# Kernel tuning notes

Hardware: AMD Instinct MI355X
Metric: run time of the kernel (lower is better)

Reference implementation:

```python
import jax, jax.numpy as jnp
import numpy as np

EPS = 1e-5
INIT_PERSIST = 0.5

def _layernorm(x):
    mu = jnp.mean(x, axis=-1, keepdims=True)
    var = jnp.var(x, axis=-1, keepdims=True)
    return (x - mu) / jnp.sqrt(var + EPS)

def setup_inputs() -> dict:
    key = jax.random.key(0)
    k1, k2, k3, k4 = jax.random.split(key, 4)
    B, T, D, N = 8, 48, 512, 1024
    return {
        "x_seq": jax.random.normal(k1, (B, T, D), dtype=jnp.float32),
        "targets": jax.random.normal(k2, (B, T, D), dtype=jnp.float32),
        "E": jax.random.normal(k3, (D, N), dtype=jnp.float32) * 0.1,
        "Dy": jax.random.normal(k4, (N, D), dtype=jnp.float32) * 0.1,
        "mix_param": jnp.zeros((), dtype=jnp.float32),
    }

def reference(x_seq, targets, E, Dy, mix_param):
    B, T, D = x_seq.shape
    N = E.shape[1]
    alpha = jax.nn.sigmoid(mix_param)

    # initial states: persist = 0.5*I, transition = 0
    Gp0 = jnp.broadcast_to(jnp.eye(N, dtype=x_seq.dtype) * INIT_PERSIST, (B, N, N))
    Gt0 = jnp.zeros((B, N, N), dtype=x_seq.dtype)

    # target for step t's update is targets[:, t+1]; last step has no update
    tgt_next = jnp.concatenate([targets[:, 1:, :], jnp.zeros_like(targets[:, :1, :])], axis=1)
    do_upd = jnp.arange(T) < (T - 1)  # [T] bool

    xs = (jnp.swapaxes(x_seq, 0, 1), jnp.swapaxes(tgt_next, 0, 1), do_upd)

    def step(carry, inp):
        Gp, Gt = carry
        x_t, tn_t, upd = inp
        xn = jax.nn.relu(_layernorm(x_t @ E))          # [B, N]
        r_p = jnp.einsum("bn,bnm->bm", xn, Gp)
        r_t = jnp.einsum("bn,bnm->bm", xn, Gt)
        y = jax.nn.relu((alpha * r_p + (1.0 - alpha) * r_t) @ Dy)  # [B, D]
        tn = jax.nn.relu(_layernorm(tn_t @ E))          # [B, N]
        Gt_new = jnp.maximum(Gt, 0.5 * xn[:, :, None] * tn[:, None, :])
        Gp_new = jnp.maximum(Gp, 0.5 * xn[:, :, None] * xn[:, None, :])
        Gt = jnp.where(upd, Gt_new, Gt)
        Gp = jnp.where(upd, Gp_new, Gp)
        return (Gp, Gt), y

    _, ys = jax.lax.scan(step, (Gp0, Gt0), xs)
    return jnp.swapaxes(ys, 0, 1)  # [B, T, D]
```

## Files before the change

### kernel.cpp

```cpp
#include <hip/hip_runtime.h>
#include <math.h>

#define BB 8
#define TT 48
#define DD 512
#define NN 1024

__global__ __launch_bounds__(256) void k_gemm_z(const float* __restrict__ x,
                                                const float* __restrict__ tg,
                                                const float* __restrict__ E,
                                                float* __restrict__ z_x,
                                                float* __restrict__ z_t) {
    int rt = blockIdx.x, ct = blockIdx.y;
    int tid = threadIdx.x;
    int tr = tid >> 4;
    int tc = tid & 15;
    int row0 = rt * 32;
    int col0 = ct * 64;

    __shared__ float As[32][16];
    __shared__ float Es[16][64];

    int e2 = tid * 2;
    int sr = e2 >> 4;
    int sk0 = e2 & 15;
    int gr_s = row0 + sr;
    const float* srow;
    if (gr_s < BB * TT) {
        srow = x + (size_t)gr_s * DD;
    } else {
        int s = gr_s - BB * TT + 1;
        if (s > BB * TT - 1) s = BB * TT - 1;
        srow = tg + (size_t)s * DD;
    }

    int se = tid >> 4;
    int sc0 = (tid & 15) * 4;
    const float* erow = E + col0 + sc0;

    float4 acc0 = make_float4(0.f, 0.f, 0.f, 0.f);
    float4 acc1 = make_float4(0.f, 0.f, 0.f, 0.f);

    for (int d0 = 0; d0 < DD; d0 += 16) {
        float2 xv = *reinterpret_cast<const float2*>(srow + d0 + sk0);
        float4 ev = *reinterpret_cast<const float4*>(erow + (size_t)(d0 + se) * NN);
        __syncthreads();
        As[sr][sk0] = xv.x;
        As[sr][sk0 + 1] = xv.y;
        *reinterpret_cast<float4*>(&Es[se][sc0]) = ev;
        __syncthreads();
#pragma unroll
        for (int k = 0; k < 16; k++) {
            float a0 = As[tr][k];
            float a1 = As[tr + 16][k];
            float4 e = *reinterpret_cast<const float4*>(&Es[k][tc * 4]);
            acc0.x = fmaf(a0, e.x, acc0.x);
            acc0.y = fmaf(a0, e.y, acc0.y);
            acc0.z = fmaf(a0, e.z, acc0.z);
            acc0.w = fmaf(a0, e.w, acc0.w);
            acc1.x = fmaf(a1, e.x, acc1.x);
            acc1.y = fmaf(a1, e.y, acc1.y);
            acc1.z = fmaf(a1, e.z, acc1.z);
            acc1.w = fmaf(a1, e.w, acc1.w);
        }
    }

    int gr0 = row0 + tr, gr1 = row0 + tr + 16;
    int cbase = col0 + tc * 4;
    if (gr0 < BB * TT)
        *reinterpret_cast<float4*>(z_x + (size_t)gr0 * NN + cbase) = acc0;
    else
        *reinterpret_cast<float4*>(z_t + (size_t)(gr0 - BB * TT) * NN + cbase) = acc0;
    if (gr1 < BB * TT)
        *reinterpret_cast<float4*>(z_x + (size_t)gr1 * NN + cbase) = acc1;
    else
        *reinterpret_cast<float4*>(z_t + (size_t)(gr1 - BB * TT) * NN + cbase) = acc1;
}

__global__ __launch_bounds__(256) void k_ln(const float* __restrict__ z_x,
                                            const float* __restrict__ z_t,
                                            float* __restrict__ xn,
                                            float* __restrict__ tn) {
    int bt = blockIdx.x;
    int t = bt % TT;
    int tid = threadIdx.x;
    __shared__ float rs_[256], rq_[256];

    const float* src = z_x + (size_t)bt * NN;
    float v0 = src[tid], v1 = src[tid + 256], v2 = src[tid + 512], v3 = src[tid + 768];
    rs_[tid] = v0 + v1 + v2 + v3;
    rq_[tid] = v0 * v0 + v1 * v1 + v2 * v2 + v3 * v3;
    __syncthreads();
    for (int off = 128; off > 0; off >>= 1) {
        if (tid < off) { rs_[tid] += rs_[tid + off]; rq_[tid] += rq_[tid + off]; }
        __syncthreads();
    }
    float mu = rs_[0] * (1.f / NN);
    float var = rq_[0] * (1.f / NN) - mu * mu;
    float rstd = rsqrtf(var + 1e-5f);
    float* xrow = xn + (size_t)bt * NN;
    xrow[tid]       = fmaxf((v0 - mu) * rstd, 0.f);
    xrow[tid + 256] = fmaxf((v1 - mu) * rstd, 0.f);
    xrow[tid + 512] = fmaxf((v2 - mu) * rstd, 0.f);
    xrow[tid + 768] = fmaxf((v3 - mu) * rstd, 0.f);
    __syncthreads();

    float* trow = tn + (size_t)bt * NN;
    if (t < TT - 1) {
        const float* s2 = z_t + (size_t)bt * NN;
        float u0 = s2[tid], u1 = s2[tid + 256], u2 = s2[tid + 512], u3 = s2[tid + 768];
        rs_[tid] = u0 + u1 + u2 + u3;
        rq_[tid] = u0 * u0 + u1 * u1 + u2 * u2 + u3 * u3;
        __syncthreads();
        for (int off = 128; off > 0; off >>= 1) {
            if (tid < off) { rs_[tid] += rs_[tid + off]; rq_[tid] += rq_[tid + off]; }
            __syncthreads();
        }
        float mu2 = rs_[0] * (1.f / NN);
        float var2 = rq_[0] * (1.f / NN) - mu2 * mu2;
        float r2 = rsqrtf(var2 + 1e-5f);
        trow[tid]       = fmaxf((u0 - mu2) * r2, 0.f);
        trow[tid + 256] = fmaxf((u1 - mu2) * r2, 0.f);
        trow[tid + 512] = fmaxf((u2 - mu2) * r2, 0.f);
        trow[tid + 768] = fmaxf((u3 - mu2) * r2, 0.f);
    } else {
        trow[tid] = 0.f; trow[tid + 256] = 0.f; trow[tid + 512] = 0.f; trow[tid + 768] = 0.f;
    }
}


typedef __attribute__((ext_vector_type(16))) float f16v;

#define GI(n) float g##n = (state == 0 && nc == cc && (n) == lane) ? 0.5f : 0.f;
#define REP64(X) X(0) X(1) X(2) X(3) X(4) X(5) X(6) X(7) X(8) X(9) X(10) X(11) X(12) X(13) \
    X(14) X(15) X(16) X(17) X(18) X(19) X(20) X(21) X(22) X(23) X(24) X(25) X(26) X(27) \
    X(28) X(29) X(30) X(31) X(32) X(33) X(34) X(35) X(36) X(37) X(38) X(39) X(40) X(41) \
    X(42) X(43) X(44) X(45) X(46) X(47) X(48) X(49) X(50) X(51) X(52) X(53) X(54) X(55) \
    X(56) X(57) X(58) X(59) X(60) X(61) X(62) X(63)

#define GS(W, I, n, A) { float wn_ = (W)[I]; float tmp_;                         \
    asm("v_fmac_f32 %[a], %[w], %[g]\n\t"                                        \
        "v_mul_f32 %[t], %[w], %[m]\n\t"                                         \
        "v_max_f32 %[g], %[g], %[t]"                                             \
        : [a]"+v"(A), [g]"+v"(g##n), [t]"=&v"(tmp_)                              \
        : [w]"s"(wn_), [m]"v"(mh)); }

__global__ __launch_bounds__(256)
__attribute__((amdgpu_waves_per_eu(2, 2)))
void k_sweep(const float* __restrict__ xn,
             const float* __restrict__ tn,
             float* __restrict__ r_part) {
    int bid = blockIdx.x;
    int ccg = bid & 3, nc = (bid >> 2) & 15, b = (bid >> 6) & 7, state = bid >> 9;
    int tid = threadIdx.x;
    int lane = tid & 63;
    int wid = __builtin_amdgcn_readfirstlane(tid >> 6);
    int cc = ccg * 4 + wid;
    int n0 = nc * 64;
    int col = cc * 64 + lane;

    REP64(GI)

    const float* wb  = xn + (size_t)b * TT * NN + n0;
    const float* mvb = (state ? tn : xn) + (size_t)b * TT * NN + col;
    float* rp = r_part + ((size_t)((state * 8 + b) * 16 + nc) * TT) * NN + col;

#pragma unroll 1
    for (int t = 0; t < TT; t++) {
        float mv = mvb[(size_t)t * NN];
        const float* xrow = wb + (size_t)t * NN;
        f16v w0, w1, w2, w3;
        asm volatile("s_load_dwordx16 %0, %4, 0x0\n\t"
                     "s_load_dwordx16 %1, %4, 0x40\n\t"
                     "s_load_dwordx16 %2, %4, 0x80\n\t"
                     "s_load_dwordx16 %3, %4, 0xc0\n\t"
                     "s_waitcnt lgkmcnt(0)"
                     : "=s"(w0), "=s"(w1), "=s"(w2), "=s"(w3)
                     : "s"(xrow)
                     : "memory");
        float sc = (t < TT - 1) ? 0.5f : 0.0f;
        float mh = mv * sc;
        float a0 = 0.f, a1 = 0.f, a2 = 0.f, a3 = 0.f;
        GS(w0,0,0,a0)   GS(w0,1,1,a1)   GS(w0,2,2,a2)   GS(w0,3,3,a3)
        GS(w0,4,4,a0)   GS(w0,5,5,a1)   GS(w0,6,6,a2)   GS(w0,7,7,a3)
        GS(w0,8,8,a0)   GS(w0,9,9,a1)   GS(w0,10,10,a2) GS(w0,11,11,a3)
        GS(w0,12,12,a0) GS(w0,13,13,a1) GS(w0,14,14,a2) GS(w0,15,15,a3)
        GS(w1,0,16,a0)  GS(w1,1,17,a1)  GS(w1,2,18,a2)  GS(w1,3,19,a3)
        GS(w1,4,20,a0)  GS(w1,5,21,a1)  GS(w1,6,22,a2)  GS(w1,7,23,a3)
        GS(w1,8,24,a0)  GS(w1,9,25,a1)  GS(w1,10,26,a2) GS(w1,11,27,a3)
        GS(w1,12,28,a0) GS(w1,13,29,a1) GS(w1,14,30,a2) GS(w1,15,31,a3)
        GS(w2,0,32,a0)  GS(w2,1,33,a1)  GS(w2,2,34,a2)  GS(w2,3,35,a3)
        GS(w2,4,36,a0)  GS(w2,5,37,a1)  GS(w2,6,38,a2)  GS(w2,7,39,a3)
        GS(w2,8,40,a0)  GS(w2,9,41,a1)  GS(w2,10,42,a2) GS(w2,11,43,a3)
        GS(w2,12,44,a0) GS(w2,13,45,a1) GS(w2,14,46,a2) GS(w2,15,47,a3)
        GS(w3,0,48,a0)  GS(w3,1,49,a1)  GS(w3,2,50,a2)  GS(w3,3,51,a3)
        GS(w3,4,52,a0)  GS(w3,5,53,a1)  GS(w3,6,54,a2)  GS(w3,7,55,a3)
        GS(w3,8,56,a0)  GS(w3,9,57,a1)  GS(w3,10,58,a2) GS(w3,11,59,a3)
        GS(w3,12,60,a0) GS(w3,13,61,a1) GS(w3,14,62,a2) GS(w3,15,63,a3)
        rp[(size_t)t * NN] = (a0 + a1) + (a2 + a3);
    }
}

__global__ __launch_bounds__(256) void k_y(const float* __restrict__ r_part,
                                           const float* __restrict__ Dy,
                                           const float* __restrict__ mixp,
                                           float* __restrict__ out) {
    int bb = blockIdx.x;
    int tg = bb & 15, b = bb >> 4;
    int tid = threadIdx.x;
    __shared__ float mixs[3][NN];
    float alpha = 1.f / (1.f + expf(-mixp[0]));

#pragma unroll
    for (int tt = 0; tt < 3; tt++) {
        int t = tg * 3 + tt;
        float spx = 0.f, spy = 0.f, spz = 0.f, spw = 0.f;
        float stx = 0.f, sty = 0.f, stz = 0.f, stw = 0.f;
#pragma unroll
        for (int nc = 0; nc < 16; nc++) {
            int bidp = (b * 16 + nc);
            int bidt = ((8 + b) * 16 + nc);
            float4 p = *reinterpret_cast<const float4*>(r_part + ((size_t)bidp * TT + t) * NN + tid * 4);
            float4 q = *reinterpret_cast<const float4*>(r_part + ((size_t)bidt * TT + t) * NN + tid * 4);
            spx += p.x; spy += p.y; spz += p.z; spw += p.w;
            stx += q.x; sty += q.y; stz += q.z; stw += q.w;
        }
        float4 m4;
        m4.x = alpha * spx + (1.f - alpha) * stx;
        m4.y = alpha * spy + (1.f - alpha) * sty;
        m4.z = alpha * spz + (1.f - alpha) * stz;
        m4.w = alpha * spw + (1.f - alpha) * stw;
        *reinterpret_cast<float4*>(&mixs[tt][tid * 4]) = m4;
    }
    __syncthreads();

    float acc[3][2];
#pragma unroll
    for (int tt = 0; tt < 3; tt++) { acc[tt][0] = 0.f; acc[tt][1] = 0.f; }

    for (int m = 0; m < NN; m += 4) {
        float w[3][4];
#pragma unroll
        for (int tt = 0; tt < 3; tt++) {
            float4 v = *reinterpret_cast<const float4*>(&mixs[tt][m]);
            w[tt][0] = v.x; w[tt][1] = v.y; w[tt][2] = v.z; w[tt][3] = v.w;
        }
#pragma unroll
        for (int j = 0; j < 4; j++) {
            float d0 = Dy[(size_t)(m + j) * DD + tid];
            float d1 = Dy[(size_t)(m + j) * DD + tid + 256];
#pragma unroll
            for (int tt = 0; tt < 3; tt++) {
                acc[tt][0] = fmaf(w[tt][j], d0, acc[tt][0]);
                acc[tt][1] = fmaf(w[tt][j], d1, acc[tt][1]);
            }
        }
    }
#pragma unroll
    for (int tt = 0; tt < 3; tt++) {
        int t = tg * 3 + tt;
        out[((size_t)b * TT + t) * DD + tid]       = fmaxf(acc[tt][0], 0.f);
        out[((size_t)b * TT + t) * DD + tid + 256] = fmaxf(acc[tt][1], 0.f);
    }
}

extern "C" void kernel_launch(void* const* d_in, const int* in_sizes, int n_in,
                              void* d_out, int out_size, void* d_ws, size_t ws_size,
                              hipStream_t stream) {
    const float* x    = (const float*)d_in[0];
    const float* tg   = (const float*)d_in[1];
    const float* E    = (const float*)d_in[2];
    const float* Dy   = (const float*)d_in[3];
    const float* mixp = (const float*)d_in[4];
    float* out = (float*)d_out;

    float* ws = (float*)d_ws;
    float* z_x    = ws;
    float* z_t    = z_x + (size_t)384 * 1024;
    float* xn     = z_t + (size_t)384 * 1024;
    float* tn     = xn + (size_t)384 * 1024;
    float* r_part = tn + (size_t)384 * 1024;

    k_gemm_z<<<dim3(24, 16), 256, 0, stream>>>(x, tg, E, z_x, z_t);
    k_ln<<<384, 256, 0, stream>>>(z_x, z_t, xn, tn);
    k_sweep<<<1024, 256, 0, stream>>>(xn, tn, r_part);
    k_y<<<128, 256, 0, stream>>>(r_part, Dy, mixp, out);
}
```

Before: 165.5 us.

## Split output projection into reduce-mix and tiled GEMM kernels; raise sweep occupancy

The fused k_y kernel, which ran only 128 blocks each streaming all of Dy, is replaced by two kernels. k_mix reduces the partial sums and applies the alpha mix into a workspace buffer across 384 blocks. k_y2 is a shared-memory tiled GEMM over 192 blocks that reuses Dy tiles across 16 rows. Separately, k_sweep's waves-per-EU hint goes from 2 to 4. That hint could force register spills in a kernel that keeps 64 state values in registers, and the split adds an extra launch plus a round trip through global memory.

```diff
diff --git a/kernel.cpp b/kernel.cpp
--- a/kernel.cpp
+++ b/kernel.cpp
@@ -146,7 +146,7 @@
         : [w]"s"(wn_), [m]"v"(mh)); }
 
 __global__ __launch_bounds__(256)
-__attribute__((amdgpu_waves_per_eu(2, 2)))
+__attribute__((amdgpu_waves_per_eu(4, 4)))
 void k_sweep(const float* __restrict__ xn,
              const float* __restrict__ tn,
              float* __restrict__ r_part) {
@@ -201,67 +201,74 @@
     }
 }
 
-__global__ __launch_bounds__(256) void k_y(const float* __restrict__ r_part,
-                                           const float* __restrict__ Dy,
-                                           const float* __restrict__ mixp,
-                                           float* __restrict__ out) {
-    int bb = blockIdx.x;
-    int tg = bb & 15, b = bb >> 4;
-    int tid = threadIdx.x;
-    __shared__ float mixs[3][NN];
+__global__ __launch_bounds__(256) void k_mix(const float* __restrict__ r_part,
+                                             const float* __restrict__ mixp,
+                                             float* __restrict__ mix) {
+    int bt = blockIdx.x;
+    int b = bt / TT, t = bt % TT;
+    int tid = threadIdx.x;
+    int c0 = tid * 4;
     float alpha = 1.f / (1.f + expf(-mixp[0]));
 
+    float spx = 0.f, spy = 0.f, spz = 0.f, spw = 0.f;
+    float stx = 0.f, sty = 0.f, stz = 0.f, stw = 0.f;
 #pragma unroll
-    for (int tt = 0; tt < 3; tt++) {
-        int t = tg * 3 + tt;
-        float spx = 0.f, spy = 0.f, spz = 0.f, spw = 0.f;
-        float stx = 0.f, sty = 0.f, stz = 0.f, stw = 0.f;
+    for (int nc = 0; nc < 16; nc++) {
+        int bidp = (b * 16 + nc);
+        int bidt = ((8 + b) * 16 + nc);
+        float4 p = *reinterpret_cast<const float4*>(r_part + ((size_t)bidp * TT + t) * NN + c0);
+        float4 q = *reinterpret_cast<const float4*>(r_part + ((size_t)bidt * TT + t) * NN + c0);
+        spx += p.x; spy += p.y; spz += p.z; spw += p.w;
+        stx += q.x; sty += q.y; stz += q.z; stw += q.w;
+    }
+    float4 m4;
+    m4.x = alpha * spx + (1.f - alpha) * stx;
+    m4.y = alpha * spy + (1.f - alpha) * sty;
+    m4.z = alpha * spz + (1.f - alpha) * stz;
+    m4.w = alpha * spw + (1.f - alpha) * stw;
+    *reinterpret_cast<float4*>(mix + (size_t)bt * NN + c0) = m4;
+}
+
+__global__ __launch_bounds__(256) void k_y2(const float* __restrict__ mix,
+                                            const float* __restrict__ Dy,
+                                            float* __restrict__ out) {
+    int ct = blockIdx.x;
+    int rt = blockIdx.y;
+    int tid = threadIdx.x;
+    int row0 = rt * 16;
+    int col0 = ct * 64;
+    int r = tid >> 4;
+    int tc = tid & 15;
+
+    __shared__ float As[16][16];
+    __shared__ float Ds[16][64];
+
+    int sr = tid >> 4, sk = tid & 15;
+    int se = tid >> 4, sc0 = (tid & 15) * 4;
+
+    float4 acc = make_float4(0.f, 0.f, 0.f, 0.f);
+
+    for (int m0 = 0; m0 < NN; m0 += 16) {
+        float av = mix[(size_t)(row0 + sr) * NN + m0 + sk];
+        float4 dv = *reinterpret_cast<const float4*>(Dy + (size_t)(m0 + se) * DD + col0 + sc0);
+        __syncthreads();
+        As[sr][sk] = av;
+        *reinterpret_cast<float4*>(&Ds[se][sc0]) = dv;
+        __syncthreads();
 #pragma unroll
-        for (int nc = 0; nc < 16; nc++) {
-            int bidp = (b * 16 + nc);
-            int bidt = ((8 + b) * 16 + nc);
-            float4 p = *reinterpret_cast<const float4*>(r_part + ((size_t)bidp * TT + t) * NN + tid * 4);
-            float4 q = *reinterpret_cast<const float4*>(r_part + ((size_t)bidt * TT + t) * NN + tid * 4);
-            spx += p.x; spy += p.y; spz += p.z; spw += p.w;
-            stx += q.x; sty += q.y; stz += q.z; stw += q.w;
+        for (int k = 0; k < 16; k++) {
+            float a = As[r][k];
+            float4 e = *reinterpret_cast<const float4*>(&Ds[k][tc * 4]);
+            acc.x = fmaf(a, e.x, acc.x);
+            acc.y = fmaf(a, e.y, acc.y);
+            acc.z = fmaf(a, e.z, acc.z);
+            acc.w = fmaf(a, e.w, acc.w);
         }
-        float4 m4;
-        m4.x = alpha * spx + (1.f - alpha) * stx;
-        m4.y = alpha * spy + (1.f - alpha) * sty;
-        m4.z = alpha * spz + (1.f - alpha) * stz;
-        m4.w = alpha * spw + (1.f - alpha) * stw;
-        *reinterpret_cast<float4*>(&mixs[tt][tid * 4]) = m4;
-    }
-    __syncthreads();
-
-    float acc[3][2];
-#pragma unroll
-    for (int tt = 0; tt < 3; tt++) { acc[tt][0] = 0.f; acc[tt][1] = 0.f; }
-
-    for (int m = 0; m < NN; m += 4) {
-        float w[3][4];
-#pragma unroll
-        for (int tt = 0; tt < 3; tt++) {
-            float4 v = *reinterpret_cast<const float4*>(&mixs[tt][m]);
-            w[tt][0] = v.x; w[tt][1] = v.y; w[tt][2] = v.z; w[tt][3] = v.w;
-        }
-#pragma unroll
-        for (int j = 0; j < 4; j++) {
-            float d0 = Dy[(size_t)(m + j) * DD + tid];
-            float d1 = Dy[(size_t)(m + j) * DD + tid + 256];
-#pragma unroll
-            for (int tt = 0; tt < 3; tt++) {
-                acc[tt][0] = fmaf(w[tt][j], d0, acc[tt][0]);
-                acc[tt][1] = fmaf(w[tt][j], d1, acc[tt][1]);
-            }
-        }
-    }
-#pragma unroll
-    for (int tt = 0; tt < 3; tt++) {
-        int t = tg * 3 + tt;
-        out[((size_t)b * TT + t) * DD + tid]       = fmaxf(acc[tt][0], 0.f);
-        out[((size_t)b * TT + t) * DD + tid + 256] = fmaxf(acc[tt][1], 0.f);
-    }
+    }
+
+    float4 o = make_float4(fmaxf(acc.x, 0.f), fmaxf(acc.y, 0.f),
+                           fmaxf(acc.z, 0.f), fmaxf(acc.w, 0.f));
+    *reinterpret_cast<float4*>(out + (size_t)(row0 + r) * DD + col0 + tc * 4) = o;
 }
 
 extern "C" void kernel_launch(void* const* d_in, const int* in_sizes, int n_in,
@@ -280,9 +287,11 @@
     float* xn     = z_t + (size_t)384 * 1024;
     float* tn     = xn + (size_t)384 * 1024;
     float* r_part = tn + (size_t)384 * 1024;
+    float* mixbuf = r_part + (size_t)256 * 48 * 1024;
 
     k_gemm_z<<<dim3(24, 16), 256, 0, stream>>>(x, tg, E, z_x, z_t);
     k_ln<<<384, 256, 0, stream>>>(z_x, z_t, xn, tn);
     k_sweep<<<1024, 256, 0, stream>>>(xn, tn, r_part);
-    k_y<<<128, 256, 0, stream>>>(r_part, Dy, mixp, out);
-}
+    k_mix<<<384, 256, 0, stream>>>(r_part, mixp, mixbuf);
+    k_y2<<<dim3(8, 24), 256, 0, stream>>>(mixbuf, Dy, out);
+}
```

Result: faster. 143.1 us (-13.5%).
